# Performance work log

Hardware: AMD Instinct MI355X
Metric: run time of the kernel (lower is better)

The kernel has to match this reference:

```python
import jax, jax.numpy as jnp
import numpy as np

BLOCK = 64          # block_dim
GAPS = (1, 64)      # block_dim**i for i in range(num_layers=2), input_dim=4096
N_BLOCKS = 64       # input_dim // block_dim
HID = 128           # 2 * block_dim (hidden_layers_ratio=[2])
BS = 8192
IN_DIM = 4096


def setup_inputs() -> dict:
    key = jax.random.key(0)
    kx, kw1, kw2 = jax.random.split(key, 3)
    x = jax.random.normal(kx, (BS, IN_DIM), dtype=jnp.float32)
    # one BlockResMLP per factorized layer: BlockLinear(64, 64, 128) -> ELU -> BlockLinear(64, 128, 64)
    w1 = jax.random.normal(kw1, (len(GAPS), N_BLOCKS, BLOCK, HID), dtype=jnp.float32) / np.sqrt(BLOCK)
    b1 = jnp.zeros((len(GAPS), N_BLOCKS, 1, HID), dtype=jnp.float32)
    w2 = jax.random.normal(kw2, (len(GAPS), N_BLOCKS, HID, BLOCK), dtype=jnp.float32) / np.sqrt(HID)
    b2 = jnp.zeros((len(GAPS), N_BLOCKS, 1, BLOCK), dtype=jnp.float32)
    return {"x": x, "w1": w1, "b1": b1, "w2": w2, "b2": b2}


def _facto(y, w1, b1, w2, b2):
    # BlockResMLP.forward: view(bs, n_blocks, BLOCK).transpose(0,1) -> batched block GEMMs -> residual
    bs = y.shape[0]
    z = y.reshape(bs, -1, BLOCK).transpose(1, 0, 2)              # (n_blocks, bs, BLOCK)
    h = jnp.einsum('nbd,nde->nbe', z, w1) + b1                   # BlockLinear 1 + bias
    h = jax.nn.elu(h)                                            # ELU (alpha=1)
    h = jnp.einsum('nbe,ned->nbd', h, w2) + b2                   # BlockLinear 2 + bias
    z = h + z                                                    # residual
    return z.transpose(1, 0, 2).reshape(bs, -1)


def reference(x, w1, b1, w2, b2):
    bs = x.shape[0]
    y = x
    for i, gap in enumerate(GAPS):
        # permutation shuffle: view(-1, BLOCK, gap).transpose(2,1).contiguous().view(bs,-1)
        y = y.reshape(-1, BLOCK, gap).transpose(0, 2, 1).reshape(bs, -1)
        y = _facto(y, w1[i], b1[i], w2[i], b2[i])
        # inverse shuffle: view(-1, gap, BLOCK).transpose(2,1)
        y = y.reshape(-1, gap, BLOCK).transpose(0, 2, 1).reshape(bs, -1)
    return y
```

## Files before the change

kernel.cpp:

```cpp
#include <hip/hip_runtime.h>


typedef short short8 __attribute__((ext_vector_type(8)));
typedef float floatx4 __attribute__((ext_vector_type(4)));

#define MFMA(A, B, C) __builtin_amdgcn_mfma_f32_16x16x32_bf16((A), (B), (C), 0, 0, 0)

__device__ __forceinline__ unsigned short bf16r(float f) {
  unsigned int u = __builtin_bit_cast(unsigned int, f);
  u += 0x7FFFu + ((u >> 16) & 1u);
  return (unsigned short)(u >> 16);
}
__device__ __forceinline__ float bf16f(unsigned short h) {
  unsigned int u = ((unsigned int)h) << 16;
  return __builtin_bit_cast(float, u);
}
__device__ __forceinline__ float eluf(float v) {
  return v > 0.f ? v : (__expf(v) - 1.f);
}

__global__ __launch_bounds__(256) void k0_prep(const float* __restrict__ w1,
                                               const float* __restrict__ w2,
                                               short* __restrict__ w1t,
                                               short* __restrict__ w2t) {
  int tid = blockIdx.x * 256 + threadIdx.x;
  int d  = tid & 63;
  int e  = (tid >> 6) & 127;
  int ln = tid >> 13;
  w1t[tid] = (short)bf16r(w1[((size_t)ln * 64 + d) * 128 + e]);
  int e2 = tid & 127;
  int dp = (tid >> 7) & 63;
  w2t[tid] = (short)bf16r(w2[((size_t)ln * 128 + e2) * 64 + dp]);
}

__global__ __launch_bounds__(256) void k1_layer0(
    const float* __restrict__ x,
    const short* __restrict__ w1t, const short* __restrict__ w2t,
    const float* __restrict__ b1,  const float* __restrict__ b2,
    short* __restrict__ y1) {
  __shared__ __align__(16) short hst[4][2][16][72];
  const int tid  = threadIdx.x;
  const int lane = tid & 63;
  const int wv   = tid >> 6;
  const int il   = lane & 15;
  const int q    = lane >> 4;
  const int npair   = blockIdx.x & 31;
  const int rowtile = blockIdx.x >> 5;
  const int n  = npair * 2 + (wv & 1);
  const int r0 = rowtile * 64 + (wv >> 1) * 32;

  const short* w1n = w1t + (size_t)n * 8192;
  const short* w2n = w2t + (size_t)n * 8192;
  const float* b1n = b1 + n * 128;
  const float* b2n = b2 + n * 64;

  floatx4 acc2[2][4] = {};
  for (int hh = 0; hh < 2; ++hh) {
    floatx4 acc1[2][4] = {};
#pragma unroll
    for (int ks = 0; ks < 2; ++ks) {
      short8 a[2];
#pragma unroll
      for (int Mt = 0; Mt < 2; ++Mt) {
        const float* xp = x + (size_t)(r0 + Mt * 16 + il) * 4096 + n * 64 + ks * 32 + q * 8;
        floatx4 f0 = *(const floatx4*)xp;
        floatx4 f1 = *(const floatx4*)(xp + 4);
        short8 t;
#pragma unroll
        for (int u = 0; u < 4; ++u) { t[u] = (short)bf16r(f0[u]); t[4 + u] = (short)bf16r(f1[u]); }
        a[Mt] = t;
      }
#pragma unroll
      for (int nt = 0; nt < 4; ++nt) {
        short8 b = *(const short8*)(w1n + (hh * 64 + nt * 16 + il) * 64 + ks * 32 + q * 8);
        acc1[0][nt] = MFMA(a[0], b, acc1[0][nt]);
        acc1[1][nt] = MFMA(a[1], b, acc1[1][nt]);
      }
    }
#pragma unroll
    for (int nt = 0; nt < 4; ++nt) {
      float bias = b1n[hh * 64 + nt * 16 + il];
#pragma unroll
      for (int Mt = 0; Mt < 2; ++Mt)
#pragma unroll
        for (int rg = 0; rg < 4; ++rg) {
          float v = acc1[Mt][nt][rg] + bias;
          hst[wv][Mt][q * 4 + rg][nt * 16 + il] = (short)bf16r(eluf(v));
        }
    }
    asm volatile("s_waitcnt lgkmcnt(0)" ::: "memory");
#pragma unroll
    for (int ks2 = 0; ks2 < 2; ++ks2) {
      short8 a2[2];
      a2[0] = *(const short8*)&hst[wv][0][il][ks2 * 32 + q * 8];
      a2[1] = *(const short8*)&hst[wv][1][il][ks2 * 32 + q * 8];
#pragma unroll
      for (int nt2 = 0; nt2 < 4; ++nt2) {
        short8 b = *(const short8*)(w2n + (nt2 * 16 + il) * 128 + hh * 64 + ks2 * 32 + q * 8);
        acc2[0][nt2] = MFMA(a2[0], b, acc2[0][nt2]);
        acc2[1][nt2] = MFMA(a2[1], b, acc2[1][nt2]);
      }
    }
    asm volatile("s_waitcnt lgkmcnt(0)" ::: "memory");
  }
#pragma unroll
  for (int Mt = 0; Mt < 2; ++Mt) {
    const int R0 = r0 + Mt * 16 + q * 4;
#pragma unroll
    for (int nt2 = 0; nt2 < 4; ++nt2) {
      const int j = nt2 * 16 + il;
      const float bias = b2n[j];
      float v0 = acc2[Mt][nt2][0] + bias + x[(size_t)(R0 + 0) * 4096 + n * 64 + j];
      float v1 = acc2[Mt][nt2][1] + bias + x[(size_t)(R0 + 1) * 4096 + n * 64 + j];
      float v2 = acc2[Mt][nt2][2] + bias + x[(size_t)(R0 + 2) * 4096 + n * 64 + j];
      float v3 = acc2[Mt][nt2][3] + bias + x[(size_t)(R0 + 3) * 4096 + n * 64 + j];
      uint2 pk;
      pk.x = (unsigned int)bf16r(v0) | ((unsigned int)bf16r(v1) << 16);
      pk.y = (unsigned int)bf16r(v2) | ((unsigned int)bf16r(v3) << 16);
      *(uint2*)(y1 + ((size_t)(j * 64 + n) * 8192 + R0)) = pk;
    }
  }
}

__global__ __launch_bounds__(256) void k2_layer1(
    const short* __restrict__ y1,
    const short* __restrict__ w1t, const short* __restrict__ w2t,
    const float* __restrict__ b1,  const float* __restrict__ b2,
    short* __restrict__ y2) {
  __shared__ __align__(16) short hst[4][16][72];
  const int tid  = threadIdx.x;
  const int lane = tid & 63;
  const int wv   = tid >> 6;
  const int il   = lane & 15;
  const int q    = lane >> 4;
  const int mpair   = blockIdx.x & 31;
  const int rowtile = blockIdx.x >> 5;
  const int m  = mpair * 2 + (wv & 1);
  const int r0 = rowtile * 32 + (wv >> 1) * 16;

  const short* w1m = w1t + (size_t)(64 + m) * 8192;
  const short* w2m = w2t + (size_t)(64 + m) * 8192;
  const float* b1m = b1 + (64 + m) * 128;
  const float* b2m = b2 + (64 + m) * 64;

  floatx4 acc2[4] = {};
  for (int hh = 0; hh < 2; ++hh) {
    floatx4 acc1[4] = {};
#pragma unroll
    for (int ks = 0; ks < 2; ++ks) {
      const short* zp = y1 + ((size_t)(m * 64 + ks * 32 + q * 8)) * 8192 + (r0 + il);
      short8 a;
#pragma unroll
      for (int jj = 0; jj < 8; ++jj) a[jj] = zp[(size_t)jj * 8192];
#pragma unroll
      for (int nt = 0; nt < 4; ++nt) {
        short8 b = *(const short8*)(w1m + (hh * 64 + nt * 16 + il) * 64 + ks * 32 + q * 8);
        acc1[nt] = MFMA(a, b, acc1[nt]);
      }
    }
#pragma unroll
    for (int nt = 0; nt < 4; ++nt) {
      float bias = b1m[hh * 64 + nt * 16 + il];
#pragma unroll
      for (int rg = 0; rg < 4; ++rg) {
        float v = acc1[nt][rg] + bias;
        hst[wv][q * 4 + rg][nt * 16 + il] = (short)bf16r(eluf(v));
      }
    }
    asm volatile("s_waitcnt lgkmcnt(0)" ::: "memory");
#pragma unroll
    for (int ks2 = 0; ks2 < 2; ++ks2) {
      short8 a2 = *(const short8*)&hst[wv][il][ks2 * 32 + q * 8];
#pragma unroll
      for (int nt2 = 0; nt2 < 4; ++nt2) {
        short8 b = *(const short8*)(w2m + (nt2 * 16 + il) * 128 + hh * 64 + ks2 * 32 + q * 8);
        acc2[nt2] = MFMA(a2, b, acc2[nt2]);
      }
    }
    asm volatile("s_waitcnt lgkmcnt(0)" ::: "memory");
  }
#pragma unroll
  for (int nt2 = 0; nt2 < 4; ++nt2) {
    const int j = nt2 * 16 + il;
    const float bias = b2m[j];
    const uint2 zr = *(const uint2*)(y1 + (size_t)(m * 64 + j) * 8192 + (r0 + q * 4));
    hst[wv][q * 4 + 0][j] = (short)bf16r(acc2[nt2][0] + bias + bf16f((unsigned short)(zr.x & 0xFFFF)));
    hst[wv][q * 4 + 1][j] = (short)bf16r(acc2[nt2][1] + bias + bf16f((unsigned short)(zr.x >> 16)));
    hst[wv][q * 4 + 2][j] = (short)bf16r(acc2[nt2][2] + bias + bf16f((unsigned short)(zr.y & 0xFFFF)));
    hst[wv][q * 4 + 3][j] = (short)bf16r(acc2[nt2][3] + bias + bf16f((unsigned short)(zr.y >> 16)));
  }
  asm volatile("s_waitcnt lgkmcnt(0)" ::: "memory");
  const int rr = lane & 15;
  const int iq = lane >> 4;
#pragma unroll
  for (int t = 0; t < 4; ++t) {
    const uint2 v = *(const uint2*)&hst[wv][rr][t * 16 + iq * 4];
    *(uint2*)(y2 + ((size_t)(m * 8192 + r0 + rr)) * 64 + t * 16 + iq * 4) = v;
  }
}

__global__ __launch_bounds__(256) void k3_unshuffle(
    const short* __restrict__ y2, float* __restrict__ out) {
  __shared__ __align__(16) short st[4][64][68];
  const int tid  = threadIdx.x;
  const int lane = tid & 63;
  const int wv   = tid >> 6;
  const int R    = blockIdx.x * 4 + wv;
  const int mq = lane >> 2;
  const int iq = lane & 3;
#pragma unroll
  for (int mt = 0; mt < 4; ++mt) {
#pragma unroll
    for (int it = 0; it < 4; ++it) {
      const int mm = mt * 16 + mq;
      const int i  = it * 16 + iq * 4;
      const uint2 v = *(const uint2*)(y2 + ((size_t)(mm * 8192 + R)) * 64 + i);
      *(uint2*)&st[wv][mm][i] = v;
    }
  }
  asm volatile("s_waitcnt vmcnt(0) lgkmcnt(0)" ::: "memory");
  float* orow = out + (size_t)R * 4096;
#pragma unroll 4
  for (int i = 0; i < 64; ++i) {
    orow[i * 64 + lane] = bf16f((unsigned short)st[wv][lane][i]);
  }
}

extern "C" void kernel_launch(void* const* d_in, const int* in_sizes, int n_in,
                              void* d_out, int out_size, void* d_ws, size_t ws_size,
                              hipStream_t stream) {
  const float* x  = (const float*)d_in[0];
  const float* w1 = (const float*)d_in[1];
  const float* b1 = (const float*)d_in[2];
  const float* w2 = (const float*)d_in[3];
  const float* b2 = (const float*)d_in[4];
  float* out = (float*)d_out;

  short* w1t = (short*)d_ws;
  short* w2t = w1t + (1u << 20);
  short* y1  = w2t + (1u << 20);
  short* y2  = y1 + (1ull << 25);

  hipLaunchKernelGGL(k0_prep,      dim3(4096), dim3(256), 0, stream, w1, w2, w1t, w2t);
  hipLaunchKernelGGL(k1_layer0,    dim3(4096), dim3(256), 0, stream, x, w1t, w2t, b1, b2, y1);
  hipLaunchKernelGGL(k2_layer1,    dim3(8192), dim3(256), 0, stream, y1, w1t, w2t, b1, b2, y2);
  hipLaunchKernelGGL(k3_unshuffle, dim3(2048), dim3(256), 0, stream, y2, out);
}
```

Baseline: 502.7 us.

## Tile intermediate y1 layout by 32-row chunks and stage layer-1 input through LDS

The layer-0 kernel now writes y1 in a tiled layout of 32-row chunks per (i, m) pair instead of a fully strided column-major layout, and loads its x tile once, outside the hidden-half loop. The layer-1 kernel assigns one block to each 64-row tile of a single m and loads its 64x64 input tile with wide coalesced reads. It transposes that tile into LDS, where it serves as the MFMA A operand and the residual. This replaces scattered 2-byte strided global gathers in the second layer. The cost is an extra LDS transpose and a block-wide barrier, plus more registers held for the preloaded x fragments.

```diff
diff --git a/kernel.cpp b/kernel.cpp
--- a/kernel.cpp
+++ b/kernel.cpp
@@ -54,27 +54,31 @@
   const float* b1n = b1 + n * 128;
   const float* b2n = b2 + n * 64;
 
+  short8 a[2][2];
+#pragma unroll
+  for (int Mt = 0; Mt < 2; ++Mt) {
+#pragma unroll
+    for (int ks = 0; ks < 2; ++ks) {
+      const float* xp = x + (size_t)(r0 + Mt * 16 + il) * 4096 + n * 64 + ks * 32 + q * 8;
+      floatx4 f0 = *(const floatx4*)xp;
+      floatx4 f1 = *(const floatx4*)(xp + 4);
+      short8 t;
+#pragma unroll
+      for (int u = 0; u < 4; ++u) { t[u] = (short)bf16r(f0[u]); t[4 + u] = (short)bf16r(f1[u]); }
+      a[ks][Mt] = t;
+    }
+  }
+
   floatx4 acc2[2][4] = {};
   for (int hh = 0; hh < 2; ++hh) {
     floatx4 acc1[2][4] = {};
 #pragma unroll
     for (int ks = 0; ks < 2; ++ks) {
-      short8 a[2];
-#pragma unroll
-      for (int Mt = 0; Mt < 2; ++Mt) {
-        const float* xp = x + (size_t)(r0 + Mt * 16 + il) * 4096 + n * 64 + ks * 32 + q * 8;
-        floatx4 f0 = *(const floatx4*)xp;
-        floatx4 f1 = *(const floatx4*)(xp + 4);
-        short8 t;
-#pragma unroll
-        for (int u = 0; u < 4; ++u) { t[u] = (short)bf16r(f0[u]); t[4 + u] = (short)bf16r(f1[u]); }
-        a[Mt] = t;
-      }
 #pragma unroll
       for (int nt = 0; nt < 4; ++nt) {
         short8 b = *(const short8*)(w1n + (hh * 64 + nt * 16 + il) * 64 + ks * 32 + q * 8);
-        acc1[0][nt] = MFMA(a[0], b, acc1[0][nt]);
-        acc1[1][nt] = MFMA(a[1], b, acc1[1][nt]);
+        acc1[0][nt] = MFMA(a[ks][0], b, acc1[0][nt]);
+        acc1[1][nt] = MFMA(a[ks][1], b, acc1[1][nt]);
       }
     }
 #pragma unroll
@@ -103,6 +107,7 @@
     }
     asm volatile("s_waitcnt lgkmcnt(0)" ::: "memory");
   }
+  const size_t nbase = ((size_t)(r0 >> 5) * 64 + n) * 64;
 #pragma unroll
   for (int Mt = 0; Mt < 2; ++Mt) {
     const int R0 = r0 + Mt * 16 + q * 4;
@@ -117,7 +122,7 @@
       uint2 pk;
       pk.x = (unsigned int)bf16r(v0) | ((unsigned int)bf16r(v1) << 16);
       pk.y = (unsigned int)bf16r(v2) | ((unsigned int)bf16r(v3) << 16);
-      *(uint2*)(y1 + ((size_t)(j * 64 + n) * 8192 + R0)) = pk;
+      *(uint2*)(y1 + (nbase + j) * 32 + Mt * 16 + q * 4) = pk;
     }
   }
 }
@@ -127,17 +132,32 @@
     const short* __restrict__ w1t, const short* __restrict__ w2t,
     const float* __restrict__ b1,  const float* __restrict__ b2,
     short* __restrict__ y2) {
-  __shared__ __align__(16) short hst[4][16][72];
+  __shared__ __align__(16) short zL[64][72];
+  __shared__ __align__(16) short hs[4][16][72];
   const int tid  = threadIdx.x;
   const int lane = tid & 63;
   const int wv   = tid >> 6;
   const int il   = lane & 15;
   const int q    = lane >> 4;
-  const int mpair   = blockIdx.x & 31;
-  const int rowtile = blockIdx.x >> 5;
-  const int m  = mpair * 2 + (wv & 1);
-  const int r0 = rowtile * 32 + (wv >> 1) * 16;
-
+  const int m  = blockIdx.x & 63;
+  const int R0 = (blockIdx.x >> 6) * 64;
+
+  {
+    const int i    = tid & 63;
+    const int half = tid >> 6;
+    const short* src = y1 + (((size_t)((R0 >> 5) + (half >> 1)) * 64 + i) * 64 + m) * 32 + (half & 1) * 16;
+    uint4 v0 = *(const uint4*)src;
+    uint4 v1 = *(const uint4*)(src + 8);
+    const short* p0 = (const short*)&v0;
+    const short* p1 = (const short*)&v1;
+#pragma unroll
+    for (int k = 0; k < 8; ++k) zL[half * 16 + k][i] = p0[k];
+#pragma unroll
+    for (int k = 0; k < 8; ++k) zL[half * 16 + 8 + k][i] = p1[k];
+  }
+  __syncthreads();
+
+  const int mrow = wv * 16;
   const short* w1m = w1t + (size_t)(64 + m) * 8192;
   const short* w2m = w2t + (size_t)(64 + m) * 8192;
   const float* b1m = b1 + (64 + m) * 128;
@@ -148,10 +168,7 @@
     floatx4 acc1[4] = {};
 #pragma unroll
     for (int ks = 0; ks < 2; ++ks) {
-      const short* zp = y1 + ((size_t)(m * 64 + ks * 32 + q * 8)) * 8192 + (r0 + il);
-      short8 a;
-#pragma unroll
-      for (int jj = 0; jj < 8; ++jj) a[jj] = zp[(size_t)jj * 8192];
+      short8 a = *(const short8*)&zL[mrow + il][ks * 32 + q * 8];
 #pragma unroll
       for (int nt = 0; nt < 4; ++nt) {
         short8 b = *(const short8*)(w1m + (hh * 64 + nt * 16 + il) * 64 + ks * 32 + q * 8);
@@ -163,14 +180,13 @@
       float bias = b1m[hh * 64 + nt * 16 + il];
 #pragma unroll
       for (int rg = 0; rg < 4; ++rg) {
-        float v = acc1[nt][rg] + bias;
-        hst[wv][q * 4 + rg][nt * 16 + il] = (short)bf16r(eluf(v));
+        hs[wv][q * 4 + rg][nt * 16 + il] = (short)bf16r(eluf(acc1[nt][rg] + bias));
       }
     }
     asm volatile("s_waitcnt lgkmcnt(0)" ::: "memory");
 #pragma unroll
     for (int ks2 = 0; ks2 < 2; ++ks2) {
-      short8 a2 = *(const short8*)&hst[wv][il][ks2 * 32 + q * 8];
+      short8 a2 = *(const short8*)&hs[wv][il][ks2 * 32 + q * 8];
 #pragma unroll
       for (int nt2 = 0; nt2 < 4; ++nt2) {
         short8 b = *(const short8*)(w2m + (nt2 * 16 + il) * 128 + hh * 64 + ks2 * 32 + q * 8);
@@ -183,19 +199,19 @@
   for (int nt2 = 0; nt2 < 4; ++nt2) {
     const int j = nt2 * 16 + il;
     const float bias = b2m[j];
-    const uint2 zr = *(const uint2*)(y1 + (size_t)(m * 64 + j) * 8192 + (r0 + q * 4));
-    hst[wv][q * 4 + 0][j] = (short)bf16r(acc2[nt2][0] + bias + bf16f((unsigned short)(zr.x & 0xFFFF)));
-    hst[wv][q * 4 + 1][j] = (short)bf16r(acc2[nt2][1] + bias + bf16f((unsigned short)(zr.x >> 16)));
-    hst[wv][q * 4 + 2][j] = (short)bf16r(acc2[nt2][2] + bias + bf16f((unsigned short)(zr.y & 0xFFFF)));
-    hst[wv][q * 4 + 3][j] = (short)bf16r(acc2[nt2][3] + bias + bf16f((unsigned short)(zr.y >> 16)));
+#pragma unroll
+    for (int k = 0; k < 4; ++k) {
+      float r = bf16f((unsigned short)zL[mrow + q * 4 + k][j]);
+      hs[wv][q * 4 + k][j] = (short)bf16r(acc2[nt2][k] + bias + r);
+    }
   }
   asm volatile("s_waitcnt lgkmcnt(0)" ::: "memory");
   const int rr = lane & 15;
   const int iq = lane >> 4;
 #pragma unroll
   for (int t = 0; t < 4; ++t) {
-    const uint2 v = *(const uint2*)&hst[wv][rr][t * 16 + iq * 4];
-    *(uint2*)(y2 + ((size_t)(m * 8192 + r0 + rr)) * 64 + t * 16 + iq * 4) = v;
+    const uint2 v = *(const uint2*)&hs[wv][rr][t * 16 + iq * 4];
+    *(uint2*)(y2 + ((size_t)(m * 8192 + R0 + mrow + rr)) * 64 + t * 16 + iq * 4) = v;
   }
 }
 
```

Measured after the change: 466.3 us. 7.3% less time.
